# Kernel optimization log

Measured on AMD Instinct MI355X. Metric: run time of the kernel, lower is better.

## Reference

```python
import jax, jax.numpy as jnp
import numpy as np

MAX_K = 70  # 70*5 = 350 = Linear in-features
EPS = 1e-5


def _bn(x, g, b):
    # BatchNorm1d with track_running_stats=False -> always batch stats, biased var
    m = jnp.mean(x, axis=0)
    v = jnp.mean((x - m) ** 2, axis=0)
    return (x - m) * jax.lax.rsqrt(v + EPS) * g + b


def _stack_bind(feat, ccids, n_comps):
    # Pack up to MAX_K member features per connected component: [n_comps, MAX_K*F]
    N, F = feat.shape
    order = jnp.argsort(ccids)              # stable sort by component id
    sc = ccids[order]
    sf = feat[order]
    pos = jnp.arange(N)
    is_start = jnp.concatenate([jnp.ones((1,), bool), sc[1:] != sc[:-1]])
    seg_start = jax.lax.cummax(jnp.where(is_start, pos, 0))
    rank = pos - seg_start                  # index of item within its component
    valid = rank < MAX_K
    comp_idx = jnp.where(valid, sc, n_comps)  # overflow items dropped
    rank_c = jnp.minimum(rank, MAX_K - 1)
    out = jnp.zeros((n_comps + 1, MAX_K, F), feat.dtype)
    out = out.at[comp_idx, rank_c].set(sf, mode='drop')
    return out[:n_comps].reshape(n_comps, MAX_K * F)


def setup_inputs() -> dict:
    key = jax.random.key(0)
    ks = jax.random.split(key, 8)
    N, C, B, NC = 4_000_000, 200_000, 64, 1000
    std = 0.1
    inp = {
        'item_feat': jax.random.normal(ks[0], (N, 5), jnp.float32),
        'ccids': jax.random.randint(ks[1], (N,), 0, C, jnp.int32),
        'imgid': jax.random.randint(ks[2], (C,), 0, B, jnp.int32),
        'W1': jax.random.normal(ks[3], (350, 32), jnp.float32) * std,
        'b1': jnp.zeros((32,), jnp.float32),
        'g1': jnp.ones((32,), jnp.float32),
        'be1': jnp.zeros((32,), jnp.float32),
        'W2': jax.random.normal(ks[4], (32, 64), jnp.float32) * std,
        'b2': jnp.zeros((64,), jnp.float32),
        'g2': jnp.ones((64,), jnp.float32),
        'be2': jnp.zeros((64,), jnp.float32),
        'W3': jax.random.normal(ks[5], (64, 128), jnp.float32) * std,
        'b3': jnp.zeros((128,), jnp.float32),
        'g3': jnp.ones((128,), jnp.float32),
        'be3': jnp.zeros((128,), jnp.float32),
        'W4': jax.random.normal(ks[6], (128, 256), jnp.float32) * std,
        'b4': jnp.zeros((256,), jnp.float32),
        'g4': jnp.ones((256,), jnp.float32),
        'be4': jnp.zeros((256,), jnp.float32),
        'g5': jnp.ones((256,), jnp.float32),
        'be5': jnp.zeros((256,), jnp.float32),
        'Wfc': jax.random.normal(ks[7], (256, NC), jnp.float32) * (1.0 / np.sqrt(256.0)),
        'bfc': jnp.zeros((NC,), jnp.float32),
        'n_comps': C,
        'batch_size': B,
    }
    return inp


def reference(item_feat, ccids, imgid,
              W1, b1, g1, be1, W2, b2, g2, be2,
              W3, b3, g3, be3, W4, b4, g4, be4,
              g5, be5, Wfc, bfc, n_comps, batch_size):
    x = _stack_bind(item_feat, ccids, n_comps)            # [C, 350]
    x = jax.nn.relu(_bn(x @ W1 + b1, g1, be1))
    x = jax.nn.relu(_bn(x @ W2 + b2, g2, be2))
    x = jax.nn.relu(_bn(x @ W3 + b3, g3, be3))
    x = jax.nn.relu(_bn(x @ W4 + b4, g4, be4))            # [C, 256]
    # avg_pool over components per image
    s = jax.ops.segment_sum(x, imgid, num_segments=batch_size)
    cnt = jax.ops.segment_sum(jnp.ones((x.shape[0],), x.dtype), imgid,
                              num_segments=batch_size)
    cnt = jnp.where(cnt < 1, jnp.ones_like(cnt), cnt)
    x = s / cnt[:, None]                                   # [B, 256]
    x = _bn(x, g5, be5)
    x = jax.nn.relu(x @ Wfc + bfc)                         # [B, n_classes]
    return x
```

## Files before the change

kernel.cpp:

```cpp
#include <hip/hip_runtime.h>
#include <hip/hip_bf16.h>
#include <cstdint>
#include <cstddef>

#define MAX_K 70
#define BN_EPS 1e-5f
#define KPAD 360
#define NPOOL 16
#define ACHUNK 2048
#define BCHUNK 2048
#define CCAP 3584
#define NSBMAX 2048
#define NDCOPY 64
#define DSTRIDE 1408

typedef __attribute__((ext_vector_type(4))) float f32x4;
typedef __attribute__((ext_vector_type(8))) short bf16x8;
typedef __attribute__((ext_vector_type(4))) int i32x4;

__device__ inline float loadv(const float* p, size_t i) { return p[i]; }
__device__ inline float loadv(const __hip_bfloat16* p, size_t i) {
    return __bfloat162float(p[i]);
}
__device__ inline void storev(float* p, size_t i, float v) { p[i] = v; }
__device__ inline void storev(__hip_bfloat16* p, size_t i, float v) {
    p[i] = __float2bfloat16(v);
}
__device__ inline float bf2f(unsigned short u) {
    union { unsigned int i; float f; } x; x.i = ((unsigned int)u) << 16; return x.f;
}
__device__ inline unsigned short f2bfu(float f) {
    __hip_bfloat16 h = __float2bfloat16(f);
    return *reinterpret_cast<unsigned short*>(&h);
}

__global__ __launch_bounds__(256) void hist_kernel(
    const i32x4* __restrict__ cc4, int* __restrict__ sbsize,
    const int* __restrict__ imgid, int* __restrict__ pcnt,
    int n4, int C, int cg, int nsb, int B) {
    __shared__ int h[NSBMAX];
    __shared__ int scnt[64];
    int tid = threadIdx.x;
    int nsbtot = 8 * nsb;
    for (int t = tid; t < nsbtot; t += 256) h[t] = 0;
    if (tid < B) scnt[tid] = 0;
    __syncthreads();
    int per = (n4 + gridDim.x - 1) / gridDim.x;
    int q0 = blockIdx.x * per, q1 = min(q0 + per, n4);
    for (int q = q0 + tid; q < q1; q += 256) {
        i32x4 v = cc4[q];
        #pragma unroll
        for (int e = 0; e < 4; ++e) {
            int c = v[e];
            int g = c / cg;
            int loc = c - g * cg;
            atomicAdd(&h[g * nsb + (loc >> 7)], 1);
        }
    }
    for (int i = blockIdx.x * 256 + tid; i < C; i += gridDim.x * 256)
        atomicAdd(&scnt[imgid[i]], 1);
    __syncthreads();
    for (int t = tid; t < nsbtot; t += 256) {
        int v = h[t];
        if (v) atomicAdd(&sbsize[t], v);
    }
    if (tid < B) {
        int v = scnt[tid];
        if (v) atomicAdd(&pcnt[tid], v);
    }
}

__global__ void prep_kernel(const float* __restrict__ W4,
                            const float* __restrict__ W1,
                            unsigned short* __restrict__ w4t,
                            unsigned short* __restrict__ w1t) {
    int idx = blockIdx.x * 256 + threadIdx.x;
    if (idx < 32768) {
        int n = idx >> 7, k = idx & 127;
        w4t[idx] = f2bfu(W4[k * 256 + n]);
    } else if (idx < 32768 + 32 * 352) {
        int j = idx - 32768;
        int ch = j / 352, k = j - ch * 352;
        w1t[j] = (k < 350) ? f2bfu(W1[k * 32 + ch]) : 0;
    }
}

template <int FO>
__global__ void finalize_kernel(const float* __restrict__ ds,
                                const float* __restrict__ dq,
                                const float* __restrict__ g,
                                const float* __restrict__ be,
                                float* __restrict__ aS, float* __restrict__ cS,
                                int C) {
    int ch = threadIdx.x;
    if (ch < FO) {
        float s = 0.f, q = 0.f;
        #pragma unroll
        for (int k = 0; k < NDCOPY; ++k) {
            s += ds[(size_t)k * DSTRIDE + ch];
            q += dq[(size_t)k * DSTRIDE + ch];
        }
        double m = (double)s / (double)C;
        double v = (double)q / (double)C - m * m;
        float rs = rsqrtf((float)v + BN_EPS);
        float a = g[ch] * rs;
        aS[ch] = a;
        cS[ch] = be[ch] - (float)m * a;
    }
}

__global__ __launch_bounds__(256) void scan_sb(
    const int* __restrict__ sbsize, int* __restrict__ sboff,
    int* __restrict__ sbcur, int* __restrict__ bcur,
    int nsbtot, int nsb, int N) {
    __shared__ int sc[256];
    int tid = threadIdx.x;
    int base = tid * 8;
    int v[8];
    int tsum = 0;
    #pragma unroll
    for (int e = 0; e < 8; ++e) {
        int i = base + e;
        v[e] = (i < nsbtot) ? sbsize[i] : 0;
        tsum += v[e];
    }
    sc[tid] = tsum;
    __syncthreads();
    for (int d = 1; d < 256; d <<= 1) {
        int t = (tid >= d) ? sc[tid - d] : 0;
        __syncthreads();
        sc[tid] += t;
        __syncthreads();
    }
    int run = sc[tid] - tsum;
    #pragma unroll
    for (int e = 0; e < 8; ++e) {
        int i = base + e;
        if (i < nsbtot) { sboff[i] = run; sbcur[i] = run; }
        run += v[e];
    }
    if (tid == 0) sboff[nsbtot] = N;
    __syncthreads();
    if (tid < 8) bcur[tid] = (tid * nsb < nsbtot) ? sboff[tid * nsb] : N;
}

__global__ __launch_bounds__(256) void bucketA_kernel(
    const int* __restrict__ ccids, const float* __restrict__ feat,
    int* __restrict__ bcur, i32x4* __restrict__ bstage, int N, int cg) {
    __shared__ int scnt[8], scur[8];
    int tid = threadIdx.x;
    int base = blockIdx.x * ACHUNK;
    if (tid < 8) scnt[tid] = 0;
    __syncthreads();
    int myg[8], myloc[8];
    #pragma unroll
    for (int k = 0; k < 8; ++k) {
        int i = base + k * 256 + tid;
        int g = -1, loc = 0;
        if (i < N) {
            int c = ccids[i];
            g = c / cg;
            loc = c - g * cg;
            atomicAdd(&scnt[g], 1);
        }
        myg[k] = g; myloc[k] = loc;
    }
    __syncthreads();
    if (tid < 8) scur[tid] = atomicAdd(&bcur[tid], scnt[tid]);
    __syncthreads();
    #pragma unroll
    for (int k = 0; k < 8; ++k) {
        int i = base + k * 256 + tid;
        if (i < N) {
            const float* fp = &feat[(size_t)i * 5];
            float f0 = fp[0], f1 = fp[1], f2 = fp[2], f3 = fp[3], f4 = fp[4];
            int slot = atomicAdd(&scur[myg[k]], 1);
            i32x4 r;
            r[0] = i;
            r[1] = (int)(((unsigned)f2bfu(f0)) | (((unsigned)f2bfu(f1)) << 16));
            r[2] = (int)(((unsigned)f2bfu(f2)) | (((unsigned)f2bfu(f3)) << 16));
            r[3] = (int)(((unsigned)f2bfu(f4)) | (((unsigned)myloc[k]) << 16));
            bstage[slot] = r;
        }
    }
}

__global__ __launch_bounds__(256) void bucketB2_kernel(
    const i32x4* __restrict__ bstage, const int* __restrict__ sboff,
    int* __restrict__ sbcur, i32x4* __restrict__ bstage2,
    int N, int C, int cg, int nsb) {
    __shared__ int scntA[256];
    __shared__ int spref[256];
    __shared__ int scur[256];
    __shared__ int sgbase[256];
    __shared__ unsigned char sbof[BCHUNK];
    __shared__ i32x4 stage2[BCHUNK];
    int tid = threadIdx.x;
    int g  = blockIdx.x & 7;
    int k  = blockIdx.x >> 3;
    int nk = gridDim.x >> 3;
    int bs = sboff[g * nsb];
    int be = sboff[(g + 1) * nsb];
    for (int cbase = bs + k * BCHUNK; cbase < be; cbase += nk * BCHUNK) {
        int cnt_ = min(BCHUNK, be - cbase);
        scntA[tid] = 0;
        __syncthreads();
        i32x4 it[8]; int sb[8];
        #pragma unroll
        for (int u = 0; u < 8; ++u) {
            int t = u * 256 + tid;
            sb[u] = -1;
            if (t < cnt_) {
                it[u] = bstage[cbase + t];
                int loc = (int)(((unsigned)it[u][3]) >> 16);
                sb[u] = loc >> 7;
                atomicAdd(&scntA[sb[u]], 1);
            }
        }
        __syncthreads();
        spref[tid] = scntA[tid];
        __syncthreads();
        for (int d = 1; d < 256; d <<= 1) {
            int t = (tid >= d) ? spref[tid - d] : 0;
            __syncthreads();
            spref[tid] += t;
            __syncthreads();
        }
        int excl = spref[tid] - scntA[tid];
        __syncthreads();
        spref[tid] = excl;
        scur[tid] = 0;
        if (tid < nsb && scntA[tid] > 0)
            sgbase[tid] = atomicAdd(&sbcur[g * nsb + tid], scntA[tid]);
        __syncthreads();
        #pragma unroll
        for (int u = 0; u < 8; ++u) {
            if (sb[u] >= 0) {
                int w = atomicAdd(&scur[sb[u]], 1);
                int pos = spref[sb[u]] + w;
                stage2[pos] = it[u];
                sbof[pos] = (unsigned char)sb[u];
            }
        }
        __syncthreads();
        for (int t = tid; t < cnt_; t += 256) {
            int s = sbof[t];
            bstage2[sgbase[s] + (t - spref[s])] = stage2[t];
        }
        __syncthreads();
    }
}

__global__ __launch_bounds__(256) void bucketC_kernel(
    const i32x4* __restrict__ bstage2, const int* __restrict__ sboff,
    i32x4* __restrict__ srec, int* __restrict__ cnt, int* __restrict__ off,
    int N, int C, int cg, int nsb) {
    int g  = blockIdx.x >> 8;
    int sb = blockIdx.x & 255;
    if (sb >= nsb) return;
    int c0 = g * cg + sb * 128;
    if (c0 >= C) return;
    int gend = min(g * cg + cg, C);
    int c1 = min(c0 + 128, gend);
    int nc = c1 - c0;
    int gsb = g * nsb + sb;
    int p0 = sboff[gsb];
    int p1 = sboff[gsb + 1];
    int count = p1 - p0;
    int tid = threadIdx.x;
    __shared__ i32x4 stg[CCAP];
    __shared__ int ccnt[128], cpref[128], ccur[128];
    if (count <= CCAP) {
        if (tid < 128) ccnt[tid] = 0;
        __syncthreads();
        for (int t = tid; t < count; t += 256) {
            int loc = (int)(((unsigned)bstage2[p0 + t][3]) >> 16);
            atomicAdd(&ccnt[loc - sb * 128], 1);
        }
        __syncthreads();
        if (tid < 128) cpref[tid] = ccnt[tid];
        __syncthreads();
        for (int d = 1; d < 128; d <<= 1) {
            int t = (tid >= d && tid < 128) ? cpref[tid - d] : 0;
            __syncthreads();
            if (tid < 128) cpref[tid] += t;
            __syncthreads();
        }
        if (tid < 128) { cpref[tid] -= ccnt[tid]; ccur[tid] = 0; }
        __syncthreads();
        if (tid < nc) {
            cnt[c0 + tid] = ccnt[tid];
            off[c0 + tid] = p0 + cpref[tid];
        }
        for (int t = tid; t < count; t += 256) {
            i32x4 r = bstage2[p0 + t];
            int cl = (int)(((unsigned)r[3]) >> 16) - sb * 128;
            int w = atomicAdd(&ccur[cl], 1);
            stg[cpref[cl] + w] = r;
        }
        __syncthreads();
        for (int t = tid; t < count; t += 256) {
            i32x4 r = stg[t];
            int cl = (int)(((unsigned)r[3]) >> 16) - sb * 128;
            int b0 = cpref[cl], cn = ccnt[cl];
            int my = r[0];
            int rk = 0;
            for (int j = 0; j < cn; ++j)
                rk += (stg[b0 + j][0] < my) ? 1 : 0;
            srec[p0 + b0 + rk] = r;
        }
    } else {
        for (int cl = tid; cl < nc; cl += 256) {
            int myloc = sb * 128 + cl;
            int cc = 0, bb = 0;
            for (int j = 0; j < count; ++j) {
                int ol = (int)(((unsigned)bstage2[p0 + j][3]) >> 16);
                cc += (ol == myloc) ? 1 : 0;
                bb += (ol < myloc) ? 1 : 0;
            }
            cnt[c0 + cl] = cc;
            off[c0 + cl] = p0 + bb;
        }
        for (int t = tid; t < count; t += 256) {
            i32x4 r = bstage2[p0 + t];
            int myloc = (int)(((unsigned)r[3]) >> 16);
            int my = r[0];
            int rk = 0, base = 0;
            for (int j = 0; j < count; ++j) {
                i32x4 o = bstage2[p0 + j];
                int ol = (int)(((unsigned)o[3]) >> 16);
                if (ol == myloc) rk += (o[0] < my) ? 1 : 0;
                else if (ol < myloc) base += 1;
            }
            srec[p0 + base + rk] = r;
        }
    }
}

__global__ __launch_bounds__(256) void layer1_mfma(
    const i32x4* __restrict__ srec, const int* __restrict__ cnt,
    const int* __restrict__ off,
    const unsigned short* __restrict__ w1t, const float* __restrict__ b1,
    float* __restrict__ z1, float* __restrict__ dsum,
    float* __restrict__ dsq, int C) {
    __shared__ unsigned short xtile[4][16][KPAD];
    __shared__ float sps[4][32], spq[4][32];
    int tid  = threadIdx.x;
    int w    = tid >> 6;
    int lane = tid & 63;
    int cbase = blockIdx.x * 64 + w * 16;

    unsigned int* xz = (unsigned int*)&xtile[w][0][0];
    for (int t = lane; t < 16 * (KPAD / 2); t += 64) xz[t] = 0u;

    int myc = 0, myo = 0;
    {
        int comp = cbase + (lane & 15);
        if (comp < C) { myc = cnt[comp]; myo = off[comp]; }
    }
    int fl[16], bs[16];
    #pragma unroll
    for (int s = 0; s < 16; ++s) {
        fl[s] = __shfl(myc, s);
        bs[s] = __shfl(myo, s);
    }
    __syncthreads();
    #pragma unroll
    for (int s = 0; s < 16; ++s) {
        int lim = min(fl[s], MAX_K);
        for (int e = lane; e < lim; e += 64) {
            i32x4 r = srec[bs[s] + e];
            unsigned short* xp = &xtile[w][s][e * 5];
            unsigned int y1 = (unsigned int)r[1];
            unsigned int y2 = (unsigned int)r[2];
            unsigned int y3 = (unsigned int)r[3];
            xp[0] = (unsigned short)(y1 & 0xffff);
            xp[1] = (unsigned short)(y1 >> 16);
            xp[2] = (unsigned short)(y2 & 0xffff);
            xp[3] = (unsigned short)(y2 >> 16);
            xp[4] = (unsigned short)(y3 & 0xffff);
        }
    }
    __syncthreads();

    int l15 = lane & 15, l4 = lane >> 4;
    f32x4 acc0 = {0.f, 0.f, 0.f, 0.f};
    f32x4 acc1 = {0.f, 0.f, 0.f, 0.f};
    const unsigned short* xbase = &xtile[w][l15][0];
    #pragma unroll
    for (int ks = 0; ks < 11; ++ks) {
        int k0 = ks * 32 + l4 * 8;
        bf16x8 a  = *(const bf16x8*)&xbase[k0];
        bf16x8 b0 = *(const bf16x8*)&w1t[(size_t)l15 * 352 + k0];
        bf16x8 bv = *(const bf16x8*)&w1t[(size_t)(16 + l15) * 352 + k0];
        acc0 = __builtin_amdgcn_mfma_f32_16x16x32_bf16(a, b0, acc0, 0, 0, 0);
        acc1 = __builtin_amdgcn_mfma_f32_16x16x32_bf16(a, bv, acc1, 0, 0, 0);
    }
    float bias0 = b1[l15];
    float bias1 = b1[16 + l15];
    float s0 = 0.f, q0 = 0.f, s1 = 0.f, q1 = 0.f;
    #pragma unroll
    for (int r = 0; r < 4; ++r) {
        int comp = cbase + l4 * 4 + r;
        if (comp < C) {
            float z0 = acc0[r] + bias0;
            float z1v = acc1[r] + bias1;
            z1[(size_t)comp * 32 + l15]      = z0;
            z1[(size_t)comp * 32 + 16 + l15] = z1v;
            s0 += z0; q0 += z0 * z0;
            s1 += z1v; q1 += z1v * z1v;
        }
    }
    s0 += __shfl_xor(s0, 16); s0 += __shfl_xor(s0, 32);
    q0 += __shfl_xor(q0, 16); q0 += __shfl_xor(q0, 32);
    s1 += __shfl_xor(s1, 16); s1 += __shfl_xor(s1, 32);
    q1 += __shfl_xor(q1, 16); q1 += __shfl_xor(q1, 32);
    if (lane < 16) {
        sps[w][l15] = s0;      spq[w][l15] = q0;
        sps[w][16 + l15] = s1; spq[w][16 + l15] = q1;
    }
    __syncthreads();
    if (tid < 32) {
        float s = sps[0][tid] + sps[1][tid] + sps[2][tid] + sps[3][tid];
        float q = spq[0][tid] + spq[1][tid] + spq[2][tid] + spq[3][tid];
        size_t cb = (size_t)(blockIdx.x & (NDCOPY - 1)) * DSTRIDE;
        unsafeAtomicAdd(&dsum[cb + tid], s);
        unsafeAtomicAdd(&dsq[cb + tid],  q);
    }
}

template <typename TI, typename TO, int FI, int FO, int CT, int RT>
__global__ __launch_bounds__(256) void layer_kernel(
    const TI* __restrict__ zin, const float* __restrict__ W,
    const float* __restrict__ bias,
    const float* __restrict__ aS, const float* __restrict__ cS,
    TO* __restrict__ zout,
    float* __restrict__ dsO, float* __restrict__ dqO, int C) {
    constexpr int CHG  = FO / CT;
    constexpr int NSUB = 256 / CHG;
    constexpr int R    = NSUB * RT;
    __shared__ float h[R][FI + 1];
    __shared__ float sps[NSUB * FO];
    __shared__ float spq[NSUB * FO];
    __shared__ float aSs[FI], cSs[FI];
    int tid = threadIdx.x;
    int c0 = blockIdx.x * R;
    if (tid < FI) { aSs[tid] = aS[tid]; cSs[tid] = cS[tid]; }
    __syncthreads();
    for (int t = tid; t < R * FI; t += 256) {
        int r = t / FI, k = t % FI;
        int c = c0 + r;
        float v = (c < C) ? loadv(zin, (size_t)c * FI + k) : 0.f;
        h[r][k] = fmaxf(fmaf(aSs[k], v, cSs[k]), 0.f);
    }
    __syncthreads();
    int cg  = tid % CHG;
    int sub = tid / CHG;
    int chbase = cg * CT;
    float acc[RT][CT];
    #pragma unroll
    for (int i = 0; i < RT; ++i)
        #pragma unroll
        for (int j = 0; j < CT; ++j) acc[i][j] = 0.f;
    for (int k = 0; k < FI; ++k) {
        float wv[CT];
        #pragma unroll
        for (int j4 = 0; j4 < CT; j4 += 4) {
            const float4 wq = *reinterpret_cast<const float4*>(
                &W[(size_t)k * FO + chbase + j4]);
            wv[j4 + 0] = wq.x; wv[j4 + 1] = wq.y;
            wv[j4 + 2] = wq.z; wv[j4 + 3] = wq.w;
        }
        #pragma unroll
        for (int i = 0; i < RT; ++i) {
            float hv = h[sub * RT + i][k];
            #pragma unroll
            for (int j = 0; j < CT; ++j) acc[i][j] = fmaf(hv, wv[j], acc[i][j]);
        }
    }
    float ps[CT], pq[CT];
    #pragma unroll
    for (int j = 0; j < CT; ++j) { ps[j] = 0.f; pq[j] = 0.f; }
    #pragma unroll
    for (int i = 0; i < RT; ++i) {
        int c = c0 + sub * RT + i;
        if (c < C) {
            #pragma unroll
            for (int j = 0; j < CT; ++j) {
                float z = acc[i][j] + bias[chbase + j];
                storev(zout, (size_t)c * FO + chbase + j, z);
                ps[j] += z;
                pq[j] += z * z;
            }
        }
    }
    #pragma unroll
    for (int j = 0; j < CT; ++j) {
        sps[sub * FO + chbase + j] = ps[j];
        spq[sub * FO + chbase + j] = pq[j];
    }
    __syncthreads();
    if (tid < FO) {
        float s = 0.f, q = 0.f;
        #pragma unroll
        for (int s2 = 0; s2 < NSUB; ++s2) {
            s += sps[s2 * FO + tid];
            q += spq[s2 * FO + tid];
        }
        size_t cb = (size_t)(blockIdx.x & (NDCOPY - 1)) * DSTRIDE;
        unsafeAtomicAdd(&dsO[cb + tid], s);
        unsafeAtomicAdd(&dqO[cb + tid], q);
    }
}

__global__ __launch_bounds__(256, 3) void layer4_mfma(
    const __hip_bfloat16* __restrict__ z3, const unsigned short* __restrict__ w4t,
    const float* __restrict__ b4,
    const float* __restrict__ aS, const float* __restrict__ cS,
    __hip_bfloat16* __restrict__ z4,
    float* __restrict__ dsum, float* __restrict__ dsq, int C) {
    __shared__ unsigned short tile[64 * 256];
    __shared__ float sps[2][256];
    __shared__ float spq[2][256];
    __shared__ float aSs[128], cSs[128];
    int tid = threadIdx.x, wid = tid >> 6, lane = tid & 63;
    int wm = wid >> 1, wn = wid & 1;
    int c0 = blockIdx.x * 64;
    int l15 = lane & 15, l4 = lane >> 4;
    const unsigned short* z3u = (const unsigned short*)z3;
    if (tid < 128) { aSs[tid] = aS[tid]; cSs[tid] = cS[tid]; }
    __syncthreads();

    bf16x8 afrag[2][4];
    int rowA0 = c0 + wm * 32 + l15;
    #pragma unroll
    for (int ks = 0; ks < 4; ++ks) {
        int k0 = ks * 32 + l4 * 8;
        #pragma unroll
        for (int mi = 0; mi < 2; ++mi) {
            int r = rowA0 + mi * 16;
            int rc = (r < C) ? r : (C - 1);
            bf16x8 raw = *(const bf16x8*)&z3u[(size_t)rc * 128 + k0];
            bf16x8 af;
            #pragma unroll
            for (int j = 0; j < 8; ++j) {
                float v = bf2f((unsigned short)raw[j]);
                float hx = fmaxf(fmaf(aSs[k0 + j], v, cSs[k0 + j]), 0.f);
                af[j] = (short)f2bfu((r < C) ? hx : 0.f);
            }
            afrag[mi][ks] = af;
        }
    }

    #pragma unroll
    for (int nh = 0; nh < 2; ++nh) {
        f32x4 acc[2][4];
        #pragma unroll
        for (int mi = 0; mi < 2; ++mi)
            #pragma unroll
            for (int ni = 0; ni < 4; ++ni)
                acc[mi][ni] = (f32x4){0.f, 0.f, 0.f, 0.f};
        #pragma unroll
        for (int ks = 0; ks < 4; ++ks) {
            int k0 = ks * 32 + l4 * 8;
            bf16x8 bfrag[4];
            #pragma unroll
            for (int ni = 0; ni < 4; ++ni) {
                int n = wn * 128 + nh * 64 + ni * 16 + l15;
                bfrag[ni] = *(const bf16x8*)&w4t[(size_t)n * 128 + k0];
            }
            #pragma unroll
            for (int mi = 0; mi < 2; ++mi)
                #pragma unroll
                for (int ni = 0; ni < 4; ++ni)
                    acc[mi][ni] = __builtin_amdgcn_mfma_f32_16x16x32_bf16(
                        afrag[mi][ks], bfrag[ni], acc[mi][ni], 0, 0, 0);
        }
        #pragma unroll
        for (int ni = 0; ni < 4; ++ni) {
            int col = wn * 128 + nh * 64 + ni * 16 + l15;
            float bv = b4[col];
            float s = 0.f, q = 0.f;
            #pragma unroll
            for (int mi = 0; mi < 2; ++mi) {
                #pragma unroll
                for (int r = 0; r < 4; ++r) {
                    int lrow = wm * 32 + mi * 16 + l4 * 4 + r;
                    float z = acc[mi][ni][r] + bv;
                    tile[lrow * 256 + col] = f2bfu(z);
                    if (c0 + lrow < C) { s += z; q += z * z; }
                }
            }
            s += __shfl_xor(s, 16); s += __shfl_xor(s, 32);
            q += __shfl_xor(q, 16); q += __shfl_xor(q, 32);
            if (lane < 16) { sps[wm][col] = s; spq[wm][col] = q; }
        }
    }
    __syncthreads();
    if (tid < 256) {
        float s = sps[0][tid] + sps[1][tid];
        float q = spq[0][tid] + spq[1][tid];
        size_t cb = (size_t)(blockIdx.x & (NDCOPY - 1)) * DSTRIDE;
        unsafeAtomicAdd(&dsum[cb + tid], s);
        unsafeAtomicAdd(&dsq[cb + tid],  q);
    }
    unsigned short* z4u = (unsigned short*)z4;
    #pragma unroll
    for (int k = 0; k < 8; ++k) {
        int ch = k * 256 + tid;
        int lrow = ch >> 5;
        int ccol = (ch & 31) * 8;
        if (c0 + lrow < C)
            *(bf16x8*)&z4u[(size_t)(c0 + lrow) * 256 + ccol] =
                *(bf16x8*)&tile[lrow * 256 + ccol];
    }
}

__global__ __launch_bounds__(256) void pool_kernel(
    const __hip_bfloat16* __restrict__ z4, const int* __restrict__ imgid,
    const float* __restrict__ aS, const float* __restrict__ cS,
    float* __restrict__ pool, int C, int B) {
    __shared__ float spool[64 * 256];
    int tid = threadIdx.x;
    int nb = B * 256;
    for (int t = tid; t < nb; t += 256) spool[t] = 0.f;
    __syncthreads();
    float a = aS[tid], cc = cS[tid];
    int per  = (C + gridDim.x - 1) / gridDim.x;
    int cbeg = blockIdx.x * per;
    int cend = min(cbeg + per, C);
    int c = cbeg;
    for (; c + 16 <= cend; c += 16) {
        float v[16];
        int im[16];
        #pragma unroll
        for (int u = 0; u < 16; ++u) {
            im[u] = imgid[c + u];
            v[u] = loadv(z4, (size_t)(c + u) * 256 + tid);
        }
        #pragma unroll
        for (int u = 0; u < 16; ++u) {
            float hv = fmaxf(fmaf(a, v[u], cc), 0.f);
            spool[im[u] * 256 + tid] += hv;
        }
    }
    for (; c < cend; ++c) {
        int img = imgid[c];
        float v = loadv(z4, (size_t)c * 256 + tid);
        float hv = fmaxf(fmaf(a, v, cc), 0.f);
        spool[img * 256 + tid] += hv;
    }
    __syncthreads();
    float* dst = pool + (size_t)(blockIdx.x & (NPOOL - 1)) * nb;
    int start = ((int)blockIdx.x * 2048) % nb;
    for (int t0 = 0; t0 < nb; t0 += 256) {
        int t = (start + t0 + tid) % nb;
        unsafeAtomicAdd(&dst[t], spool[t]);
    }
}

__global__ void bn5_kernel(const float* __restrict__ pool,
                           const int* __restrict__ pcnt,
                           const float* __restrict__ g5,
                           const float* __restrict__ be5,
                           float* __restrict__ y, int B) {
    int ch = threadIdx.x;
    int nb = B * 256;
    double s = 0.0, s2 = 0.0;
    float vals[64];
    for (int b = 0; b < B; ++b) {
        float v = 0.f;
        #pragma unroll
        for (int k = 0; k < NPOOL; ++k) v += pool[k * nb + b * 256 + ch];
        float c = (float)pcnt[b]; if (c < 1.f) c = 1.f;
        v /= c;
        vals[b] = v;
        s += (double)v; s2 += (double)v * (double)v;
    }
    double m = s / (double)B;
    double var = s2 / (double)B - m * m;
    float rs = rsqrtf((float)var + BN_EPS);
    float a = g5[ch] * rs;
    float cc = be5[ch] - (float)m * a;
    for (int b = 0; b < B; ++b)
        y[b * 256 + ch] = fmaf(a, vals[b], cc);
}

__global__ __launch_bounds__(256) void fc_kernel(
    const float* __restrict__ y, const float* __restrict__ Wfc,
    const float* __restrict__ bfc, float* __restrict__ out, int NC) {
    int b = blockIdx.y;
    int ch = blockIdx.x * 256 + threadIdx.x;
    __shared__ float sy[256];
    sy[threadIdx.x] = y[b * 256 + threadIdx.x];
    __syncthreads();
    if (ch < NC) {
        float acc = bfc[ch];
        for (int k = 0; k < 256; ++k)
            acc = fmaf(sy[k], Wfc[(size_t)k * NC + ch], acc);
        out[(size_t)b * NC + ch] = fmaxf(acc, 0.f);
    }
}

extern "C" void kernel_launch(void* const* d_in, const int* in_sizes, int n_in,
                              void* d_out, int out_size, void* d_ws,
                              size_t ws_size, hipStream_t stream) {
    const float* item_feat = (const float*)d_in[0];
    const int*   ccids     = (const int*)d_in[1];
    const int*   imgid     = (const int*)d_in[2];
    const float* W1  = (const float*)d_in[3];
    const float* b1  = (const float*)d_in[4];
    const float* g1  = (const float*)d_in[5];
    const float* be1 = (const float*)d_in[6];
    const float* W2  = (const float*)d_in[7];
    const float* b2  = (const float*)d_in[8];
    const float* g2  = (const float*)d_in[9];
    const float* be2 = (const float*)d_in[10];
    const float* W3  = (const float*)d_in[11];
    const float* b3  = (const float*)d_in[12];
    const float* g3  = (const float*)d_in[13];
    const float* be3 = (const float*)d_in[14];
    const float* W4  = (const float*)d_in[15];
    const float* b4  = (const float*)d_in[16];
    const float* g4  = (const float*)d_in[17];
    const float* be4 = (const float*)d_in[18];
    const float* g5  = (const float*)d_in[19];
    const float* be5 = (const float*)d_in[20];
    const float* Wfc = (const float*)d_in[21];
    const float* bfc = (const float*)d_in[22];
    float* out = (float*)d_out;

    const int N  = in_sizes[1];
    const int C  = in_sizes[2];
    const int NC = in_sizes[22];
    const int B  = out_size / NC;

    uint8_t* ws = (uint8_t*)d_ws;
    size_t off_ = 0;
    auto alloc = [&](size_t bytes) -> void* {
        void* p = (void*)(ws + off_);
        off_ += (bytes + 255) & ~(size_t)255;
        return p;
    };
    int*    sbsize = (int*)alloc((size_t)NSBMAX * 4);
    float*  fstats = (float*)alloc((size_t)NDCOPY * DSTRIDE * 4);
    int*    pcnt   = (int*)alloc((size_t)B * 4);
    float*  pool   = (float*)alloc((size_t)NPOOL * B * 256 * 4);
    size_t zeroBytes = off_;
    float*  y      = (float*)alloc((size_t)B * 256 * 4);
    float*  scales = (float*)alloc((size_t)(32 + 64 + 128 + 256) * 2 * 4);
    int*    cnt    = (int*)alloc((size_t)C * 4);
    int*    off    = (int*)alloc((size_t)C * 4);
    int*    sboff  = (int*)alloc((size_t)(NSBMAX + 1) * 4);
    int*    sbcur  = (int*)alloc((size_t)NSBMAX * 4);
    int*    bcur   = (int*)alloc((size_t)8 * 4);
    unsigned short* w4t = (unsigned short*)alloc((size_t)256 * 128 * 2);
    unsigned short* w1t = (unsigned short*)alloc((size_t)32 * 352 * 2);
    void* regionA = alloc((size_t)N * 16);
    void* regionB = alloc((size_t)C * 256 * 2);
    (void)ws_size;

    i32x4*           bstage  = (i32x4*)regionB;
    i32x4*           bstage2 = (i32x4*)regionA;
    i32x4*           srec    = (i32x4*)regionB;
    float*           z1      = (float*)regionA;
    __hip_bfloat16*  z3      = (__hip_bfloat16*)regionA;
    __hip_bfloat16*  z2      = (__hip_bfloat16*)regionB;
    __hip_bfloat16*  z4      = (__hip_bfloat16*)regionB;

    float *ds1 = fstats +   0, *dq1 = fstats +  32;
    float *ds2 = fstats +  64, *dq2 = fstats + 128;
    float *ds3 = fstats + 192, *dq3 = fstats + 320;
    float *ds4 = fstats + 448, *dq4 = fstats + 704;
    float *aS1 = scales +   0, *cS1 = scales +  32;
    float *aS2 = scales +  64, *cS2 = scales + 128;
    float *aS3 = scales + 192, *cS3 = scales + 320;
    float *aS4 = scales + 448, *cS4 = scales + 704;

    const int cg     = (C + 7) / 8;
    const int nsb    = (cg + 127) / 128;
    const int nsbtot = 8 * nsb;

    hipMemsetAsync(ws, 0, zeroBytes, stream);
    hist_kernel<<<512, 256, 0, stream>>>((const i32x4*)ccids, sbsize,
                                         imgid, pcnt, N / 4, C, cg, nsb, B);
    prep_kernel<<<172, 256, 0, stream>>>(W4, W1, w4t, w1t);
    scan_sb<<<1, 256, 0, stream>>>(sbsize, sboff, sbcur, bcur, nsbtot, nsb, N);
    bucketA_kernel<<<(N + ACHUNK - 1) / ACHUNK, 256, 0, stream>>>(
        ccids, item_feat, bcur, bstage, N, cg);
    bucketB2_kernel<<<1960, 256, 0, stream>>>(bstage, sboff, sbcur, bstage2,
                                              N, C, cg, nsb);
    bucketC_kernel<<<8 * 256, 256, 0, stream>>>(bstage2, sboff, srec,
                                                cnt, off, N, C, cg, nsb);

    layer1_mfma<<<(C + 63) / 64, 256, 0, stream>>>(srec, cnt, off,
                                                   w1t, b1, z1, ds1, dq1, C);
    finalize_kernel<32><<<1, 32, 0, stream>>>(ds1, dq1, g1, be1, aS1, cS1, C);

    layer_kernel<float, __hip_bfloat16, 32, 64, 4, 8>
        <<<(C + 127) / 128, 256, 0, stream>>>(z1, W2, b2, aS1, cS1,
                                              z2, ds2, dq2, C);
    finalize_kernel<64><<<1, 64, 0, stream>>>(ds2, dq2, g2, be2, aS2, cS2, C);

    layer_kernel<__hip_bfloat16, __hip_bfloat16, 64, 128, 4, 8>
        <<<(C + 63) / 64, 256, 0, stream>>>(z2, W3, b3, aS2, cS2,
                                            z3, ds3, dq3, C);
    finalize_kernel<128><<<1, 128, 0, stream>>>(ds3, dq3, g3, be3, aS3, cS3, C);

    layer4_mfma<<<(C + 63) / 64, 256, 0, stream>>>(z3, w4t, b4, aS3, cS3,
                                                   z4, ds4, dq4, C);
    finalize_kernel<256><<<1, 256, 0, stream>>>(ds4, dq4, g4, be4, aS4, cS4, C);

    pool_kernel<<<512, 256, 0, stream>>>(z4, imgid, aS4, cS4, pool, C, B);
    bn5_kernel<<<1, 256, 0, stream>>>(pool, pcnt, g5, be5, y, B);

    dim3 fcg((NC + 255) / 256, B);
    fc_kernel<<<fcg, 256, 0, stream>>>(y, Wfc, bfc, out, NC);
}
```

Measured before the change: 559.3 us.

## Port layer 3 to bf16 MFMA, store z1 as bf16, swizzle output tiles

Replaces the scalar FMA layer_kernel for the 64->128 layer with an MFMA kernel. It uses a pre-transposed bf16 copy of W3 made in prep_kernel and fuses BN+ReLU of the previous layer into the A-fragment load. The layer-1 output z1 is now stored as bf16 instead of fp32, which halves its write and read traffic. The LDS staging tiles in layers 3 and 4 get an XOR swizzle to reduce bank conflicts. Costs include less precision in z1 and the layer-3 inputs, plus one more prep pass over W3.

```diff
diff --git a/kernel.cpp b/kernel.cpp
--- a/kernel.cpp
+++ b/kernel.cpp
@@ -72,8 +72,10 @@
 
 __global__ void prep_kernel(const float* __restrict__ W4,
                             const float* __restrict__ W1,
+                            const float* __restrict__ W3,
                             unsigned short* __restrict__ w4t,
-                            unsigned short* __restrict__ w1t) {
+                            unsigned short* __restrict__ w1t,
+                            unsigned short* __restrict__ w3t) {
     int idx = blockIdx.x * 256 + threadIdx.x;
     if (idx < 32768) {
         int n = idx >> 7, k = idx & 127;
@@ -82,6 +84,10 @@
         int j = idx - 32768;
         int ch = j / 352, k = j - ch * 352;
         w1t[j] = (k < 350) ? f2bfu(W1[k * 32 + ch]) : 0;
+    } else if (idx < 32768 + 32 * 352 + 128 * 64) {
+        int j = idx - (32768 + 32 * 352);
+        int n = j >> 6, k = j & 63;
+        w3t[j] = f2bfu(W3[k * 128 + n]);
     }
 }
 
@@ -341,7 +347,7 @@
     const i32x4* __restrict__ srec, const int* __restrict__ cnt,
     const int* __restrict__ off,
     const unsigned short* __restrict__ w1t, const float* __restrict__ b1,
-    float* __restrict__ z1, float* __restrict__ dsum,
+    __hip_bfloat16* __restrict__ z1, float* __restrict__ dsum,
     float* __restrict__ dsq, int C) {
     __shared__ unsigned short xtile[4][16][KPAD];
     __shared__ float sps[4][32], spq[4][32];
@@ -405,8 +411,8 @@
         if (comp < C) {
             float z0 = acc0[r] + bias0;
             float z1v = acc1[r] + bias1;
-            z1[(size_t)comp * 32 + l15]      = z0;
-            z1[(size_t)comp * 32 + 16 + l15] = z1v;
+            storev(z1, (size_t)comp * 32 + l15, z0);
+            storev(z1, (size_t)comp * 32 + 16 + l15, z1v);
             s0 += z0; q0 += z0 * z0;
             s1 += z1v; q1 += z1v * z1v;
         }
@@ -513,6 +519,107 @@
     }
 }
 
+__global__ __launch_bounds__(256, 3) void layer3_mfma(
+    const __hip_bfloat16* __restrict__ z2, const unsigned short* __restrict__ w3t,
+    const float* __restrict__ b3,
+    const float* __restrict__ aS, const float* __restrict__ cS,
+    __hip_bfloat16* __restrict__ z3,
+    float* __restrict__ dsum, float* __restrict__ dsq, int C) {
+    __shared__ unsigned short tile[64 * 128];
+    __shared__ float sps[2][128];
+    __shared__ float spq[2][128];
+    __shared__ float aSs[64], cSs[64];
+    int tid = threadIdx.x, wid = tid >> 6, lane = tid & 63;
+    int wm = wid >> 1, wn = wid & 1;
+    int c0 = blockIdx.x * 64;
+    int l15 = lane & 15, l4 = lane >> 4;
+    const unsigned short* z2u = (const unsigned short*)z2;
+    if (tid < 64) { aSs[tid] = aS[tid]; cSs[tid] = cS[tid]; }
+    __syncthreads();
+
+    bf16x8 afrag[2][2];
+    int rowA0 = c0 + wm * 32 + l15;
+    #pragma unroll
+    for (int ks = 0; ks < 2; ++ks) {
+        int k0 = ks * 32 + l4 * 8;
+        #pragma unroll
+        for (int mi = 0; mi < 2; ++mi) {
+            int r = rowA0 + mi * 16;
+            int rc = (r < C) ? r : (C - 1);
+            bf16x8 raw = *(const bf16x8*)&z2u[(size_t)rc * 64 + k0];
+            bf16x8 af;
+            #pragma unroll
+            for (int j = 0; j < 8; ++j) {
+                float v = bf2f((unsigned short)raw[j]);
+                float hx = fmaxf(fmaf(aSs[k0 + j], v, cSs[k0 + j]), 0.f);
+                af[j] = (short)f2bfu((r < C) ? hx : 0.f);
+            }
+            afrag[mi][ks] = af;
+        }
+    }
+
+    f32x4 acc[2][4];
+    #pragma unroll
+    for (int mi = 0; mi < 2; ++mi)
+        #pragma unroll
+        for (int ni = 0; ni < 4; ++ni)
+            acc[mi][ni] = (f32x4){0.f, 0.f, 0.f, 0.f};
+    #pragma unroll
+    for (int ks = 0; ks < 2; ++ks) {
+        int k0 = ks * 32 + l4 * 8;
+        bf16x8 bfrag[4];
+        #pragma unroll
+        for (int ni = 0; ni < 4; ++ni) {
+            int n = wn * 64 + ni * 16 + l15;
+            bfrag[ni] = *(const bf16x8*)&w3t[(size_t)n * 64 + k0];
+        }
+        #pragma unroll
+        for (int mi = 0; mi < 2; ++mi)
+            #pragma unroll
+            for (int ni = 0; ni < 4; ++ni)
+                acc[mi][ni] = __builtin_amdgcn_mfma_f32_16x16x32_bf16(
+                    afrag[mi][ks], bfrag[ni], acc[mi][ni], 0, 0, 0);
+    }
+    #pragma unroll
+    for (int ni = 0; ni < 4; ++ni) {
+        int col = wn * 64 + ni * 16 + l15;
+        float bv = b3[col];
+        float s = 0.f, q = 0.f;
+        #pragma unroll
+        for (int mi = 0; mi < 2; ++mi) {
+            #pragma unroll
+            for (int r = 0; r < 4; ++r) {
+                int lrow = wm * 32 + mi * 16 + l4 * 4 + r;
+                float z = acc[mi][ni][r] + bv;
+                int sc = (col & 7) + 8 * ((col >> 3) ^ ((lrow >> 2) & 7));
+                tile[lrow * 128 + sc] = f2bfu(z);
+                if (c0 + lrow < C) { s += z; q += z * z; }
+            }
+        }
+        s += __shfl_xor(s, 16); s += __shfl_xor(s, 32);
+        q += __shfl_xor(q, 16); q += __shfl_xor(q, 32);
+        if (lane < 16) { sps[wm][col] = s; spq[wm][col] = q; }
+    }
+    __syncthreads();
+    if (tid < 128) {
+        float s = sps[0][tid] + sps[1][tid];
+        float q = spq[0][tid] + spq[1][tid];
+        size_t cb = (size_t)(blockIdx.x & (NDCOPY - 1)) * DSTRIDE;
+        unsafeAtomicAdd(&dsum[cb + tid], s);
+        unsafeAtomicAdd(&dsq[cb + tid],  q);
+    }
+    unsigned short* z3u = (unsigned short*)z3;
+    #pragma unroll
+    for (int k = 0; k < 4; ++k) {
+        int ch = k * 256 + tid;
+        int lrow = ch >> 4;
+        int c8 = ch & 15;
+        if (c0 + lrow < C)
+            *(bf16x8*)&z3u[(size_t)(c0 + lrow) * 128 + c8 * 8] =
+                *(bf16x8*)&tile[lrow * 128 + 8 * (c8 ^ ((lrow >> 2) & 7))];
+    }
+}
+
 __global__ __launch_bounds__(256, 3) void layer4_mfma(
     const __hip_bfloat16* __restrict__ z3, const unsigned short* __restrict__ w4t,
     const float* __restrict__ b4,
@@ -587,7 +694,8 @@
                 for (int r = 0; r < 4; ++r) {
                     int lrow = wm * 32 + mi * 16 + l4 * 4 + r;
                     float z = acc[mi][ni][r] + bv;
-                    tile[lrow * 256 + col] = f2bfu(z);
+                    int sc = (col & 7) + 8 * ((col >> 3) ^ ((lrow >> 2) & 7));
+                    tile[lrow * 256 + sc] = f2bfu(z);
                     if (c0 + lrow < C) { s += z; q += z * z; }
                 }
             }
@@ -609,10 +717,10 @@
     for (int k = 0; k < 8; ++k) {
         int ch = k * 256 + tid;
         int lrow = ch >> 5;
-        int ccol = (ch & 31) * 8;
+        int c8 = ch & 31;
         if (c0 + lrow < C)
-            *(bf16x8*)&z4u[(size_t)(c0 + lrow) * 256 + ccol] =
-                *(bf16x8*)&tile[lrow * 256 + ccol];
+            *(bf16x8*)&z4u[(size_t)(c0 + lrow) * 256 + c8 * 8] =
+                *(bf16x8*)&tile[lrow * 256 + 8 * (c8 ^ ((lrow >> 2) & 7))];
     }
 }
 
@@ -756,6 +864,7 @@
     int*    bcur   = (int*)alloc((size_t)8 * 4);
     unsigned short* w4t = (unsigned short*)alloc((size_t)256 * 128 * 2);
     unsigned short* w1t = (unsigned short*)alloc((size_t)32 * 352 * 2);
+    unsigned short* w3t = (unsigned short*)alloc((size_t)128 * 64 * 2);
     void* regionA = alloc((size_t)N * 16);
     void* regionB = alloc((size_t)C * 256 * 2);
     (void)ws_size;
@@ -763,7 +872,7 @@
     i32x4*           bstage  = (i32x4*)regionB;
     i32x4*           bstage2 = (i32x4*)regionA;
     i32x4*           srec    = (i32x4*)regionB;
-    float*           z1      = (float*)regionA;
+    __hip_bfloat16*  z1      = (__hip_bfloat16*)regionA;
     __hip_bfloat16*  z3      = (__hip_bfloat16*)regionA;
     __hip_bfloat16*  z2      = (__hip_bfloat16*)regionB;
     __hip_bfloat16*  z4      = (__hip_bfloat16*)regionB;
@@ -784,7 +893,7 @@
     hipMemsetAsync(ws, 0, zeroBytes, stream);
     hist_kernel<<<512, 256, 0, stream>>>((const i32x4*)ccids, sbsize,
                                          imgid, pcnt, N / 4, C, cg, nsb, B);
-    prep_kernel<<<172, 256, 0, stream>>>(W4, W1, w4t, w1t);
+    prep_kernel<<<205, 256, 0, stream>>>(W4, W1, W3, w4t, w1t, w3t);
     scan_sb<<<1, 256, 0, stream>>>(sbsize, sboff, sbcur, bcur, nsbtot, nsb, N);
     bucketA_kernel<<<(N + ACHUNK - 1) / ACHUNK, 256, 0, stream>>>(
         ccids, item_feat, bcur, bstage, N, cg);
@@ -797,14 +906,13 @@
                                                    w1t, b1, z1, ds1, dq1, C);
     finalize_kernel<32><<<1, 32, 0, stream>>>(ds1, dq1, g1, be1, aS1, cS1, C);
 
-    layer_kernel<float, __hip_bfloat16, 32, 64, 4, 8>
+    layer_kernel<__hip_bfloat16, __hip_bfloat16, 32, 64, 4, 8>
         <<<(C + 127) / 128, 256, 0, stream>>>(z1, W2, b2, aS1, cS1,
                                               z2, ds2, dq2, C);
     finalize_kernel<64><<<1, 64, 0, stream>>>(ds2, dq2, g2, be2, aS2, cS2, C);
 
-    layer_kernel<__hip_bfloat16, __hip_bfloat16, 64, 128, 4, 8>
-        <<<(C + 63) / 64, 256, 0, stream>>>(z2, W3, b3, aS2, cS2,
-                                            z3, ds3, dq3, C);
+    layer3_mfma<<<(C + 63) / 64, 256, 0, stream>>>(z2, w3t, b3, aS2, cS2,
+                                                   z3, ds3, dq3, C);
     finalize_kernel<128><<<1, 128, 0, stream>>>(ds3, dq3, g3, be3, aS3, cS3, C);
 
     layer4_mfma<<<(C + 63) / 64, 256, 0, stream>>>(z3, w4t, b4, aS3, cS3,
```

Result: faster. 525.1 us, median of 3 (-6.1%).
